# Kernel tuning notes

Measured on AMD Instinct MI355X. Metric: run time of the kernel, lower is better.

Reference implementation:

```python
import jax, jax.numpy as jnp
import numpy as np
import math

IMG_CHL = 1024
L_CHL = 512
N_PTS = 4096  # pinned by nn.LayerNorm(4096)
H = 256
W = 256
HEADS = 4
VOXEL = 1.0 / 256.0
PC_MIN = 0.0
BEV_STRIDE = 1.0
LN_EPS = 1e-5


def setup_inputs() -> dict:
    key = jax.random.key(0)
    ks = jax.random.split(key, 6)
    point_features = jax.random.normal(ks[0], (1, L_CHL, N_PTS), jnp.float32)
    kp = jax.random.uniform(ks[1], (N_PTS, 4), dtype=jnp.float32)
    keypoints = kp.at[:, 0].set(0.0)  # batch index column = 0 (batch_size=1)
    bev_features = jax.random.normal(ks[2], (1, IMG_CHL, H, W), jnp.float32)
    conv_L_w = jax.random.normal(ks[3], (L_CHL, L_CHL), jnp.float32) * 0.02
    conv_L_b = jnp.zeros((L_CHL,), jnp.float32)
    img_head_w = jax.random.normal(ks[4], (HEADS, L_CHL, IMG_CHL), jnp.float32) * 0.02
    img_head_b = jnp.zeros((HEADS, L_CHL), jnp.float32)
    ln_w = jnp.ones((N_PTS,), jnp.float32)
    ln_b = jnp.zeros((N_PTS,), jnp.float32)
    conv_fusion_w = jax.random.normal(ks[5], (L_CHL, L_CHL), jnp.float32) * 0.02
    conv_fusion_b = jnp.zeros((L_CHL,), jnp.float32)
    return {
        "point_features": point_features,
        "keypoints": keypoints,
        "bev_features": bev_features,
        "conv_L_w": conv_L_w,
        "conv_L_b": conv_L_b,
        "img_head_w": img_head_w,
        "img_head_b": img_head_b,
        "ln_w": ln_w,
        "ln_b": ln_b,
        "conv_fusion_w": conv_fusion_w,
        "conv_fusion_b": conv_fusion_b,
    }


def _bilinear_interpolate(im, x, y):
    """im: (H, W, C); x, y: (N,). Mirrors bilinear_interpolate_torch (clamped corners)."""
    x0 = jnp.clip(jnp.floor(x).astype(jnp.int32), 0, im.shape[1] - 1)
    x1 = jnp.clip(jnp.floor(x).astype(jnp.int32) + 1, 0, im.shape[1] - 1)
    y0 = jnp.clip(jnp.floor(y).astype(jnp.int32), 0, im.shape[0] - 1)
    y1 = jnp.clip(jnp.floor(y).astype(jnp.int32) + 1, 0, im.shape[0] - 1)
    Ia = im[y0, x0]  # (N, C)
    Ib = im[y1, x0]
    Ic = im[y0, x1]
    Id = im[y1, x1]
    x0f, x1f = x0.astype(x.dtype), x1.astype(x.dtype)
    y0f, y1f = y0.astype(y.dtype), y1.astype(y.dtype)
    wa = (x1f - x) * (y1f - y)
    wb = (x1f - x) * (y - y0f)
    wc = (x - x0f) * (y1f - y)
    wd = (x - x0f) * (y - y0f)
    return Ia * wa[:, None] + Ib * wb[:, None] + Ic * wc[:, None] + Id * wd[:, None]


def reference(point_features, keypoints, bev_features, conv_L_w, conv_L_b,
              img_head_w, img_head_b, ln_w, ln_b, conv_fusion_w, conv_fusion_b):
    # --- interpolate_from_bev_features (batch_size=1, all keypoints in batch 0) ---
    x_idxs = (keypoints[:, 1] - PC_MIN) / VOXEL / BEV_STRIDE
    y_idxs = (keypoints[:, 2] - PC_MIN) / VOXEL / BEV_STRIDE
    im = jnp.transpose(bev_features[0], (1, 2, 0))  # (H, W, C)
    point_bev = _bilinear_interpolate(im, x_idxs, y_idxs)  # (N, IMG_CHL)
    img_features = point_bev.T[None]  # (1, IMG_CHL, N)

    # --- Fusion_Conv_att ---
    # 1x1 Conv1d == channel matmul
    L_query = jnp.einsum('oc,bcn->bon', conv_L_w, point_features) + conv_L_b[None, :, None]  # (1, L, N)
    keys = jnp.einsum('hoc,bcn->hbon', img_head_w, img_features) + img_head_b[:, None, :, None]  # (4, 1, L, N)
    dk = L_CHL
    score = jnp.sum(keys * L_query[None], axis=2)[:, 0, :] / math.sqrt(dk)  # (4, N)
    weightmap = jax.nn.softmax(score, axis=0)[None]  # (1, 4, N) softmax over heads
    z = jnp.einsum('hn,hln->ln', weightmap[0], keys[:, 0])[None]  # (1, L, N)

    t = z + L_query
    mu = jnp.mean(t, axis=-1, keepdims=True)
    var = jnp.mean((t - mu) ** 2, axis=-1, keepdims=True)
    t = (t - mu) / jnp.sqrt(var + LN_EPS) * ln_w + ln_b  # LayerNorm over the 4096 point axis

    fusion_features = jnp.einsum('oc,bcn->bon', conv_fusion_w, t) + conv_fusion_b[None, :, None]
    return fusion_features, weightmap
```

## Files before the change

### kernel.cpp

```cpp
#include <hip/hip_runtime.h>

typedef unsigned short u16;
typedef unsigned int   u32;

typedef short s16x8 __attribute__((ext_vector_type(8)));
typedef float f32x4 __attribute__((ext_vector_type(4)));

__device__ __forceinline__ float b2f(u16 u) {
    u32 x = ((u32)u) << 16;
    float f;
    __builtin_memcpy(&f, &x, 4);
    return f;
}

__device__ __forceinline__ u16 f2b(float f) {
    u32 x;
    __builtin_memcpy(&x, &f, 4);
    u32 r = (x + 0x7fffu + ((x >> 16) & 1u)) >> 16;
    return (u16)r;
}

__global__ void prep_points(const float* __restrict__ kp,
                            int4* __restrict__ pts_off,
                            float4* __restrict__ pts_w,
                            int* __restrict__ perm) {
    __shared__ int cnt[256];
    __shared__ int base[256];
    const int t = threadIdx.x;
    cnt[t] = 0;
    __syncthreads();
    int buck[16];
    #pragma unroll
    for (int j = 0; j < 16; j++) {
        const int n = j * 256 + t;
        const float x = kp[n * 4 + 1] * 256.0f;
        const float y = kp[n * 4 + 2] * 256.0f;
        const int x0 = min(max((int)floorf(x), 0), 255);
        const int y0 = min(max((int)floorf(y), 0), 255);
        const int b = (y0 >> 3) * 8 + (x0 >> 5);
        buck[j] = b;
        atomicAdd(&cnt[b], 1);
    }
    __syncthreads();
    if (t == 0) {
        int s = 0;
        for (int i = 0; i < 256; i++) { base[i] = s; s += cnt[i]; }
    }
    __syncthreads();
    cnt[t] = 0;
    __syncthreads();
    #pragma unroll
    for (int j = 0; j < 16; j++) {
        const int n = j * 256 + t;
        const float x = kp[n * 4 + 1] * 256.0f;
        const float y = kp[n * 4 + 2] * 256.0f;
        const float xf = floorf(x), yf = floorf(y);
        const int x0 = min(max((int)xf, 0), 255);
        const int x1 = min(max((int)xf + 1, 0), 255);
        const int y0 = min(max((int)yf, 0), 255);
        const int y1 = min(max((int)yf + 1, 0), 255);
        const float x0f = (float)x0, x1f = (float)x1;
        const float y0f = (float)y0, y1f = (float)y1;
        float4 w;
        w.x = (x1f - x) * (y1f - y);
        w.y = (x1f - x) * (y - y0f);
        w.z = (x - x0f) * (y1f - y);
        w.w = (x - x0f) * (y - y0f);
        int4 o;
        o.x = y0 * 256 + x0;
        o.y = y1 * 256 + x0;
        o.z = y0 * 256 + x1;
        o.w = y1 * 256 + x1;
        const int b = buck[j];
        const int pos = base[b] + atomicAdd(&cnt[b], 1);
        perm[pos] = n;
        pts_off[pos] = o;
        pts_w[pos] = w;
    }
}

__global__ __launch_bounds__(256) void interp_sorted(const float* __restrict__ bev,
                                                     const int4* __restrict__ pts_off,
                                                     const float4* __restrict__ pts_w,
                                                     u16* __restrict__ img) {
    const int c = blockIdx.x;
    const float* plane = bev + (size_t)c * 65536;
    const int t = threadIdx.x;
    #pragma unroll
    for (int j = 0; j < 16; j++) {
        const int i = j * 256 + t;
        const int4 o = pts_off[i];
        const float4 w = pts_w[i];
        const float v = plane[o.x] * w.x + plane[o.y] * w.y +
                        plane[o.z] * w.z + plane[o.w] * w.w;
        img[(size_t)c * 4096 + i] = f2b(v);
    }
}

__global__ void convert_params(const float* clw, const float* ihw, const float* cfw,
                               const float* clb, const float* ihb,
                               const float* lnw, const float* lnb, const float* cfb,
                               u16* __restrict__ canon) {
    const int total = 2632704;
    for (int i = blockIdx.x * 256 + threadIdx.x; i < total; i += gridDim.x * 256) {
        const float* src; int off;
        if (i < 262144)       { src = clw; off = i; }
        else if (i < 2359296) { src = ihw; off = i - 262144; }
        else if (i < 2621440) { src = cfw; off = i - 2359296; }
        else if (i < 2621952) { src = clb; off = i - 2621440; }
        else if (i < 2624000) { src = ihb; off = i - 2621952; }
        else if (i < 2628096) { src = lnw; off = i - 2624000; }
        else if (i < 2632192) { src = lnb; off = i - 2628096; }
        else                  { src = cfb; off = i - 2632192; }
        canon[i] = f2b(src[off]);
    }
}

template <int ISF>
__global__ void transpose_any(const void* __restrict__ in, u16* __restrict__ out,
                              int R, int C, const int* __restrict__ perm) {
    __shared__ u16 tile[64][65];
    const int t = threadIdx.x;
    const int r0 = blockIdx.y * 64, c0 = blockIdx.x * 64;
    #pragma unroll
    for (int i = 0; i < 16; i++) {
        int idx = i * 256 + t;
        int r = idx >> 6, c = idx & 63;
        tile[r][c] = ISF ? f2b(((const float*)in)[(size_t)(r0 + r) * C + c0 + c])
                         : ((const u16*)in)[(size_t)(r0 + r) * C + c0 + c];
    }
    __syncthreads();
    #pragma unroll
    for (int i = 0; i < 16; i++) {
        int idx = i * 256 + t;
        int c = idx >> 6, r = idx & 63;
        int row = perm ? perm[c0 + c] : (c0 + c);
        out[(size_t)row * R + r0 + r] = tile[r][c];
    }
}

template <int OB>
__global__ __launch_bounds__(256) void gemm_bt(const u16* __restrict__ A,
                                               const u16* __restrict__ BT,
                                               const u16* __restrict__ bias,
                                               void* __restrict__ Cout,
                                               int M, int N, int K) {
    __shared__ __align__(16) u16 As[128 * 40];
    __shared__ __align__(16) u16 Bs[128 * 40];
    const int tid = threadIdx.x;
    const int lane = tid & 63;
    const int w = tid >> 6;
    const int m0 = blockIdx.y * 128;
    const int n0 = blockIdx.x * 128;
    const int wm = (w >> 1) * 64;
    const int wn = (w & 1) * 64;

    f32x4 acc[4][4] = {};

    for (int k0 = 0; k0 < K; k0 += 32) {
        __syncthreads();
        #pragma unroll
        for (int i = 0; i < 2; i++) {
            int s = i * 256 + tid;
            int row = s >> 2, kc = s & 3;
            *(uint4*)&As[row * 40 + kc * 8] =
                *(const uint4*)&A[(size_t)(m0 + row) * K + k0 + kc * 8];
            *(uint4*)&Bs[row * 40 + kc * 8] =
                *(const uint4*)&BT[(size_t)(n0 + row) * K + k0 + kc * 8];
        }
        __syncthreads();

        const int q = lane >> 4, r = lane & 15;
        s16x8 af[4], bfr[4];
        #pragma unroll
        for (int mt = 0; mt < 4; mt++)
            af[mt] = *(const s16x8*)&As[(wm + mt * 16 + r) * 40 + q * 8];
        #pragma unroll
        for (int nt = 0; nt < 4; nt++)
            bfr[nt] = *(const s16x8*)&Bs[(wn + nt * 16 + r) * 40 + q * 8];
        #pragma unroll
        for (int mt = 0; mt < 4; mt++)
            #pragma unroll
            for (int nt = 0; nt < 4; nt++)
                acc[mt][nt] = __builtin_amdgcn_mfma_f32_16x16x32_bf16(
                    af[mt], bfr[nt], acc[mt][nt], 0, 0, 0);
    }

    const int q = lane >> 4, cn = lane & 15;
    #pragma unroll
    for (int mt = 0; mt < 4; mt++) {
        #pragma unroll
        for (int i = 0; i < 4; i++) {
            int gm = m0 + wm + mt * 16 + q * 4 + i;
            float bv = b2f(bias[gm]);
            #pragma unroll
            for (int nt = 0; nt < 4; nt++) {
                int gn = n0 + wn + nt * 16 + cn;
                float v = acc[mt][nt][i] + bv;
                if (OB)
                    ((u16*)Cout)[(size_t)gm * N + gn] = f2b(v);
                else
                    ((float*)Cout)[(size_t)gm * N + gn] = v;
            }
        }
    }
}

__global__ void score_partial(const u16* __restrict__ keys,
                              const float* __restrict__ lq,
                              float* __restrict__ spart) {
    __shared__ float red[4][4][64];
    const int nl = threadIdx.x & 63;
    const int ls = threadIdx.x >> 6;
    const int n = blockIdx.x * 64 + nl;
    const int lbase = blockIdx.y * 128 + ls * 32;
    float acc[4] = {0.f, 0.f, 0.f, 0.f};
    for (int i = 0; i < 32; i++) {
        const int l = lbase + i;
        const float qv = lq[l * 4096 + n];
        #pragma unroll
        for (int h = 0; h < 4; h++)
            acc[h] += b2f(keys[(size_t)(h * 512 + l) * 4096 + n]) * qv;
    }
    #pragma unroll
    for (int h = 0; h < 4; h++) red[h][ls][nl] = acc[h];
    __syncthreads();
    if (threadIdx.x < 64) {
        #pragma unroll
        for (int h = 0; h < 4; h++) {
            float s = red[h][0][nl] + red[h][1][nl] + red[h][2][nl] + red[h][3][nl];
            spart[(size_t)(blockIdx.y * 4 + h) * 4096 + n] = s;
        }
    }
}

__global__ void score_finalize(const float* __restrict__ spart,
                               float* __restrict__ wm_ws,
                               float* __restrict__ out) {
    const int n = blockIdx.x * 256 + threadIdx.x;
    const float scale = 0.044194173824159216f;
    float s[4];
    #pragma unroll
    for (int h = 0; h < 4; h++) {
        float v = 0.f;
        #pragma unroll
        for (int lc = 0; lc < 4; lc++) v += spart[(size_t)(lc * 4 + h) * 4096 + n];
        s[h] = v * scale;
    }
    float mx = fmaxf(fmaxf(s[0], s[1]), fmaxf(s[2], s[3]));
    float e[4], sum = 0.f;
    #pragma unroll
    for (int h = 0; h < 4; h++) { e[h] = expf(s[h] - mx); sum += e[h]; }
    const float inv = 1.0f / sum;
    #pragma unroll
    for (int h = 0; h < 4; h++) {
        float wv = e[h] * inv;
        wm_ws[h * 4096 + n] = wv;
        out[2097152 + (size_t)h * 4096 + n] = wv;
    }
}

__global__ void compute_t(const u16* __restrict__ keys,
                          const float* __restrict__ lq,
                          const float* __restrict__ wm_ws,
                          float* __restrict__ tbuf) {
    const int n = blockIdx.x * 256 + threadIdx.x;
    const int l = blockIdx.y;
    float t = lq[l * 4096 + n];
    #pragma unroll
    for (int h = 0; h < 4; h++)
        t += wm_ws[h * 4096 + n] * b2f(keys[(size_t)(h * 512 + l) * 4096 + n]);
    tbuf[l * 4096 + n] = t;
}

__global__ void ln_stats(const float* __restrict__ tbuf,
                         float* __restrict__ mu, float* __restrict__ rstd) {
    const int l = blockIdx.x;
    const float* row = tbuf + (size_t)l * 4096;
    float s = 0.f, ss = 0.f;
    for (int i = threadIdx.x; i < 4096; i += 256) {
        float v = row[i];
        s += v;
        ss += v * v;
    }
    for (int off = 32; off > 0; off >>= 1) {
        s += __shfl_down(s, off);
        ss += __shfl_down(ss, off);
    }
    __shared__ float bs[4], bss[4];
    const int w = threadIdx.x >> 6, lane = threadIdx.x & 63;
    if (lane == 0) { bs[w] = s; bss[w] = ss; }
    __syncthreads();
    if (threadIdx.x == 0) {
        s = bs[0] + bs[1] + bs[2] + bs[3];
        ss = bss[0] + bss[1] + bss[2] + bss[3];
        float m = s * (1.0f / 4096.0f);
        float var = ss * (1.0f / 4096.0f) - m * m;
        mu[l] = m;
        rstd[l] = rsqrtf(var + 1e-5f);
    }
}

__global__ void ln_norm_transpose(const float* __restrict__ tbuf,
                                  const float* __restrict__ mu,
                                  const float* __restrict__ rstd,
                                  const u16* __restrict__ lnw,
                                  const u16* __restrict__ lnb,
                                  u16* __restrict__ out) {
    __shared__ float tile[64][65];
    const int t = threadIdx.x;
    const int r0 = blockIdx.y * 64, c0 = blockIdx.x * 64;
    #pragma unroll
    for (int i = 0; i < 16; i++) {
        int idx = i * 256 + t;
        int r = idx >> 6, c = idx & 63;
        float v = tbuf[(size_t)(r0 + r) * 4096 + c0 + c];
        v = (v - mu[r0 + r]) * rstd[r0 + r] * b2f(lnw[c0 + c]) + b2f(lnb[c0 + c]);
        tile[r][c] = v;
    }
    __syncthreads();
    #pragma unroll
    for (int i = 0; i < 16; i++) {
        int idx = i * 256 + t;
        int c = idx >> 6, r = idx & 63;
        out[(size_t)(c0 + c) * 512 + r0 + r] = f2b(tile[r][c]);
    }
}

extern "C" void kernel_launch(void* const* d_in, const int* in_sizes, int n_in,
                              void* d_out, int out_size, void* d_ws, size_t ws_size,
                              hipStream_t stream) {
    const float* pf  = (const float*)d_in[0];
    const float* kp  = (const float*)d_in[1];
    const float* bev = (const float*)d_in[2];
    const float* clw = (const float*)d_in[3];
    const float* clb = (const float*)d_in[4];
    const float* ihw = (const float*)d_in[5];
    const float* ihb = (const float*)d_in[6];
    const float* lnw = (const float*)d_in[7];
    const float* lnb = (const float*)d_in[8];
    const float* cfw = (const float*)d_in[9];
    const float* cfb = (const float*)d_in[10];
    float* out = (float*)d_out;

    char* ws = (char*)d_ws;
    u16*    img     = (u16*)(ws + 0);
    float*  tbuf    = (float*)(ws + 0);
    u16*    imgT    = (u16*)(ws + (8ull << 20));
    float*  lq      = (float*)(ws + (8ull << 20));
    u16*    keys    = (u16*)(ws + (16ull << 20));
    u16*    pfT     = (u16*)(ws + (32ull << 20));
    u16*    tT      = (u16*)(ws + (32ull << 20));
    float*  spart   = (float*)(ws + (36ull << 20));
    float*  wm_ws   = (float*)(ws + (36ull << 20) + 262144);
    float*  mu      = (float*)(ws + (36ull << 20) + 327680);
    float*  rstd    = (float*)(ws + (36ull << 20) + 329728);
    u16*    canon   = (u16*)  (ws + (36ull << 20) + 332864);
    int4*   pts_off = (int4*) (ws + (42ull << 20));
    float4* pts_w   = (float4*)(ws + (42ull << 20) + 65536);
    int*    perm    = (int*)  (ws + (42ull << 20) + 131072);

    u16* clw_c = canon;
    u16* ihw_c = canon + 262144;
    u16* cfw_c = canon + 2359296;
    u16* clb_c = canon + 2621440;
    u16* ihb_c = canon + 2621952;
    u16* lnw_c = canon + 2624000;
    u16* lnb_c = canon + 2628096;
    u16* cfb_c = canon + 2632192;

    prep_points<<<1, 256, 0, stream>>>(kp, pts_off, pts_w, perm);
    convert_params<<<1024, 256, 0, stream>>>(clw, ihw, cfw, clb, ihb, lnw, lnb, cfb, canon);
    interp_sorted<<<1024, 256, 0, stream>>>(bev, pts_off, pts_w, img);
    transpose_any<0><<<dim3(64, 16), 256, 0, stream>>>(img, imgT, 1024, 4096, perm);
    transpose_any<1><<<dim3(64, 8), 256, 0, stream>>>(pf, pfT, 512, 4096, nullptr);
    gemm_bt<1><<<dim3(32, 16), 256, 0, stream>>>(ihw_c, imgT, ihb_c, keys, 2048, 4096, 1024);
    gemm_bt<0><<<dim3(32, 4), 256, 0, stream>>>(clw_c, pfT, clb_c, lq, 512, 4096, 512);
    score_partial<<<dim3(64, 4), 256, 0, stream>>>(keys, lq, spart);
    score_finalize<<<16, 256, 0, stream>>>(spart, wm_ws, out);
    compute_t<<<dim3(16, 512), 256, 0, stream>>>(keys, lq, wm_ws, tbuf);
    ln_stats<<<512, 256, 0, stream>>>(tbuf, mu, rstd);
    ln_norm_transpose<<<dim3(64, 8), 256, 0, stream>>>(tbuf, mu, rstd, lnw_c, lnb_c, tT);
    gemm_bt<0><<<dim3(32, 4), 256, 0, stream>>>(cfw_c, tT, cfb_c, out, 512, 4096, 512);
}
```

Measured before the change: 518.8 us.

## Fuse t computation with LayerNorm, parallel prefix scan, split interp grid

Merges compute_t, ln_stats and ln_norm into one kernel per channel row. Each row is held in registers, so the fp32 tbuf round-trip and a launch are removed; the normalized bf16 row is then transposed by the generic transpose kernel. The serial 256-element prefix sum in prep_points becomes a wave-level shuffle scan. interp_sorted is split four ways across the point axis to raise block count. The fused LN kernel has only 512 blocks and uses a 16-float register array per thread, which may limit occupancy. It also reads LN weights as fp32 rather than bf16, which slightly changes numerics.

```diff
diff --git a/kernel.cpp b/kernel.cpp
--- a/kernel.cpp
+++ b/kernel.cpp
@@ -42,9 +42,20 @@
         atomicAdd(&cnt[b], 1);
     }
     __syncthreads();
-    if (t == 0) {
-        int s = 0;
-        for (int i = 0; i < 256; i++) { base[i] = s; s += cnt[i]; }
+    if (t < 64) {
+        int a0 = cnt[t * 4], a1 = cnt[t * 4 + 1], a2 = cnt[t * 4 + 2], a3 = cnt[t * 4 + 3];
+        int tot = a0 + a1 + a2 + a3;
+        int pre = tot;
+        #pragma unroll
+        for (int off = 1; off < 64; off <<= 1) {
+            int v = __shfl_up(pre, off);
+            if (t >= off) pre += v;
+        }
+        int excl = pre - tot;
+        base[t * 4]     = excl;
+        base[t * 4 + 1] = excl + a0;
+        base[t * 4 + 2] = excl + a0 + a1;
+        base[t * 4 + 3] = excl + a0 + a1 + a2;
     }
     __syncthreads();
     cnt[t] = 0;
@@ -85,10 +96,11 @@
                                                      u16* __restrict__ img) {
     const int c = blockIdx.x;
     const float* plane = bev + (size_t)c * 65536;
+    const int base_i = blockIdx.y * 1024;
     const int t = threadIdx.x;
     #pragma unroll
-    for (int j = 0; j < 16; j++) {
-        const int i = j * 256 + t;
+    for (int j = 0; j < 4; j++) {
+        const int i = base_i + j * 256 + t;
         const int4 o = pts_off[i];
         const float4 w = pts_w[i];
         const float v = plane[o.x] * w.x + plane[o.y] * w.y +
@@ -260,26 +272,24 @@
     }
 }
 
-__global__ void compute_t(const u16* __restrict__ keys,
-                          const float* __restrict__ lq,
-                          const float* __restrict__ wm_ws,
-                          float* __restrict__ tbuf) {
-    const int n = blockIdx.x * 256 + threadIdx.x;
-    const int l = blockIdx.y;
-    float t = lq[l * 4096 + n];
-    #pragma unroll
-    for (int h = 0; h < 4; h++)
-        t += wm_ws[h * 4096 + n] * b2f(keys[(size_t)(h * 512 + l) * 4096 + n]);
-    tbuf[l * 4096 + n] = t;
-}
-
-__global__ void ln_stats(const float* __restrict__ tbuf,
-                         float* __restrict__ mu, float* __restrict__ rstd) {
+__global__ __launch_bounds__(256) void compute_t_ln(const u16* __restrict__ keys,
+                                                    const float* __restrict__ lq,
+                                                    const float* __restrict__ wm_ws,
+                                                    const float* __restrict__ lnw,
+                                                    const float* __restrict__ lnb,
+                                                    u16* __restrict__ tnorm) {
     const int l = blockIdx.x;
-    const float* row = tbuf + (size_t)l * 4096;
+    const int t = threadIdx.x;
+    float tv[16];
     float s = 0.f, ss = 0.f;
-    for (int i = threadIdx.x; i < 4096; i += 256) {
-        float v = row[i];
+    #pragma unroll
+    for (int j = 0; j < 16; j++) {
+        const int n = j * 256 + t;
+        float v = lq[l * 4096 + n];
+        #pragma unroll
+        for (int h = 0; h < 4; h++)
+            v += wm_ws[h * 4096 + n] * b2f(keys[(size_t)(h * 512 + l) * 4096 + n]);
+        tv[j] = v;
         s += v;
         ss += v * v;
     }
@@ -288,42 +298,18 @@
         ss += __shfl_down(ss, off);
     }
     __shared__ float bs[4], bss[4];
-    const int w = threadIdx.x >> 6, lane = threadIdx.x & 63;
+    const int w = t >> 6, lane = t & 63;
     if (lane == 0) { bs[w] = s; bss[w] = ss; }
     __syncthreads();
-    if (threadIdx.x == 0) {
-        s = bs[0] + bs[1] + bs[2] + bs[3];
-        ss = bss[0] + bss[1] + bss[2] + bss[3];
-        float m = s * (1.0f / 4096.0f);
-        float var = ss * (1.0f / 4096.0f) - m * m;
-        mu[l] = m;
-        rstd[l] = rsqrtf(var + 1e-5f);
-    }
-}
-
-__global__ void ln_norm_transpose(const float* __restrict__ tbuf,
-                                  const float* __restrict__ mu,
-                                  const float* __restrict__ rstd,
-                                  const u16* __restrict__ lnw,
-                                  const u16* __restrict__ lnb,
-                                  u16* __restrict__ out) {
-    __shared__ float tile[64][65];
-    const int t = threadIdx.x;
-    const int r0 = blockIdx.y * 64, c0 = blockIdx.x * 64;
-    #pragma unroll
-    for (int i = 0; i < 16; i++) {
-        int idx = i * 256 + t;
-        int r = idx >> 6, c = idx & 63;
-        float v = tbuf[(size_t)(r0 + r) * 4096 + c0 + c];
-        v = (v - mu[r0 + r]) * rstd[r0 + r] * b2f(lnw[c0 + c]) + b2f(lnb[c0 + c]);
-        tile[r][c] = v;
-    }
-    __syncthreads();
-    #pragma unroll
-    for (int i = 0; i < 16; i++) {
-        int idx = i * 256 + t;
-        int c = idx >> 6, r = idx & 63;
-        out[(size_t)(c0 + c) * 512 + r0 + r] = f2b(tile[r][c]);
+    const float S = bs[0] + bs[1] + bs[2] + bs[3];
+    const float SS = bss[0] + bss[1] + bss[2] + bss[3];
+    const float mu = S * (1.0f / 4096.0f);
+    const float rstd = rsqrtf(SS * (1.0f / 4096.0f) - mu * mu + 1e-5f);
+    #pragma unroll
+    for (int j = 0; j < 16; j++) {
+        const int n = j * 256 + t;
+        const float v = (tv[j] - mu) * rstd * lnw[n] + lnb[n];
+        tnorm[(size_t)l * 4096 + n] = f2b(v);
     }
 }
 
@@ -345,7 +331,7 @@
 
     char* ws = (char*)d_ws;
     u16*    img     = (u16*)(ws + 0);
-    float*  tbuf    = (float*)(ws + 0);
+    u16*    tnorm   = (u16*)(ws + 0);
     u16*    imgT    = (u16*)(ws + (8ull << 20));
     float*  lq      = (float*)(ws + (8ull << 20));
     u16*    keys    = (u16*)(ws + (16ull << 20));
@@ -353,8 +339,6 @@
     u16*    tT      = (u16*)(ws + (32ull << 20));
     float*  spart   = (float*)(ws + (36ull << 20));
     float*  wm_ws   = (float*)(ws + (36ull << 20) + 262144);
-    float*  mu      = (float*)(ws + (36ull << 20) + 327680);
-    float*  rstd    = (float*)(ws + (36ull << 20) + 329728);
     u16*    canon   = (u16*)  (ws + (36ull << 20) + 332864);
     int4*   pts_off = (int4*) (ws + (42ull << 20));
     float4* pts_w   = (float4*)(ws + (42ull << 20) + 65536);
@@ -365,21 +349,18 @@
     u16* cfw_c = canon + 2359296;
     u16* clb_c = canon + 2621440;
     u16* ihb_c = canon + 2621952;
-    u16* lnw_c = canon + 2624000;
-    u16* lnb_c = canon + 2628096;
     u16* cfb_c = canon + 2632192;
 
     prep_points<<<1, 256, 0, stream>>>(kp, pts_off, pts_w, perm);
     convert_params<<<1024, 256, 0, stream>>>(clw, ihw, cfw, clb, ihb, lnw, lnb, cfb, canon);
-    interp_sorted<<<1024, 256, 0, stream>>>(bev, pts_off, pts_w, img);
+    interp_sorted<<<dim3(1024, 4), 256, 0, stream>>>(bev, pts_off, pts_w, img);
     transpose_any<0><<<dim3(64, 16), 256, 0, stream>>>(img, imgT, 1024, 4096, perm);
     transpose_any<1><<<dim3(64, 8), 256, 0, stream>>>(pf, pfT, 512, 4096, nullptr);
     gemm_bt<1><<<dim3(32, 16), 256, 0, stream>>>(ihw_c, imgT, ihb_c, keys, 2048, 4096, 1024);
     gemm_bt<0><<<dim3(32, 4), 256, 0, stream>>>(clw_c, pfT, clb_c, lq, 512, 4096, 512);
     score_partial<<<dim3(64, 4), 256, 0, stream>>>(keys, lq, spart);
     score_finalize<<<16, 256, 0, stream>>>(spart, wm_ws, out);
-    compute_t<<<dim3(16, 512), 256, 0, stream>>>(keys, lq, wm_ws, tbuf);
-    ln_stats<<<512, 256, 0, stream>>>(tbuf, mu, rstd);
-    ln_norm_transpose<<<dim3(64, 8), 256, 0, stream>>>(tbuf, mu, rstd, lnw_c, lnb_c, tT);
+    compute_t_ln<<<512, 256, 0, stream>>>(keys, lq, wm_ws, lnw, lnb, tnorm);
+    transpose_any<0><<<dim3(64, 8), 256, 0, stream>>>(tnorm, tT, 512, 4096, nullptr);
     gemm_bt<0><<<dim3(32, 4), 256, 0, stream>>>(cfw_c, tT, cfb_c, out, 512, 4096, 512);
 }
```

After: 511.7 us. No clear change (-1.4%).
